# Kernel tuning notes

Measured on AMD Instinct MI355X. Metric: run time of the kernel, lower is better.

Reference implementation:

```python
import jax, jax.numpy as jnp
import numpy as np

B, N, C = 32, 2248, 1024
D = 128            # bottleneck (down_size)
P = 200            # num_prompt_tokens
SCALE = D ** (-0.5)


def setup_inputs() -> dict:
    key = jax.random.key(0)
    k = jax.random.split(key, 5)
    return {
        "x": jax.random.normal(k[0], (B, N, C), dtype=jnp.float32),
        "W_down": jax.random.normal(k[1], (C, D), dtype=jnp.float32) * (C ** -0.5),
        "b_down": jax.random.normal(k[2], (D,), dtype=jnp.float32) * 0.01,
        "W_up": jax.random.normal(k[3], (D, C), dtype=jnp.float32) * (D ** -0.5),
        "b_up": jax.random.normal(k[4], (C,), dtype=jnp.float32) * 0.01,
        "gate": jnp.ones((), dtype=jnp.float32),
    }


def reference(x, W_down, b_down, W_up, b_up, gate):
    # down-projection + exact GELU (torch nn.GELU default is erf-based)
    down = jax.nn.gelu(jnp.einsum('bnc,cd->bnd', x, W_down) + b_down,
                       approximate=False)                      # [B, N, D]
    prompt_down = down[:, :P, :]                               # [B, P, D]
    token_down = down[:, P:, :]                                # [B, N-P, D]
    # prompt-token cross attention
    attn = jax.nn.softmax(
        jnp.einsum('bpd,btd->bpt', prompt_down, token_down) * SCALE, axis=-1)
    prompt_out = jnp.einsum('bpt,btd->bpd', attn, token_down)  # [B, P, D]
    combined = jnp.concatenate([prompt_out, token_down], axis=1)  # [B, N, D]
    up = jnp.einsum('bnd,dc->bnc', combined, W_up) + b_up      # [B, N, C]
    return gate * up
```

## Files before the change

kernel.cpp:

```cpp
#include <hip/hip_runtime.h>
#include <hip/hip_bf16.h>
#include <math.h>

#define B_   32
#define N_   2248
#define C_   1024
#define D_   128
#define P_   200
#define T_   2048
#define M_   (B_ * N_)
#define SCALE_ 0.08838834764831845f

typedef __bf16 bf16;
typedef __bf16 bf16x8 __attribute__((ext_vector_type(8)));
typedef __bf16 bf16x4 __attribute__((ext_vector_type(4)));
typedef float  f32x4  __attribute__((ext_vector_type(4)));
typedef unsigned int u32x4 __attribute__((ext_vector_type(4)));

#define VT_COL(dd, t) ((((((t) >> 3) ^ (((dd) >> 3) & 7)) << 3)) | ((t) & 7))

__device__ __forceinline__ void gl_lds16(const void* g, void* l) {
    __builtin_amdgcn_global_load_lds(
        (const __attribute__((address_space(1))) unsigned int*)g,
        (__attribute__((address_space(3))) unsigned int*)l,
        16, 0, 0);
}

__global__ void k_prep(const float* __restrict__ Wd, const float* __restrict__ Wu,
                       bf16* __restrict__ WtD, bf16* __restrict__ WtU) {
    int i = blockIdx.x * 256 + threadIdx.x;
    if (i >= 131072) return;
    int d = i >> 10, k = i & 1023;
    WtD[i] = (bf16)Wd[k * 128 + d];
    int c = i >> 7, e = i & 127;
    WtU[i] = (bf16)Wu[e * 1024 + c];
}

__launch_bounds__(256, 3)
__global__ void k_down(const float* __restrict__ x, const bf16* __restrict__ WtD,
                       const float* __restrict__ bd, bf16* __restrict__ down) {
    __shared__ __align__(16) char ring[3][16384];
    const int tid = threadIdx.x;
    const int lane = tid & 63, w = tid >> 6;
    const int wm = w >> 1, wn = w & 1;
    const int li = lane & 15, lg = lane >> 4;
    const int m0 = blockIdx.x * 64;

    const int cA0 = w * 2, cA1 = w * 2 + 1;
    const int ar0 = cA0 * 8 + (lane >> 3);
    const int ar1 = cA1 * 8 + (lane >> 3);
    const float* asrc0 = x + (size_t)(m0 + ar0) * C_ + ((((lane & 7) ^ (ar0 & 7)) * 16) >> 2);
    const float* asrc1 = x + (size_t)(m0 + ar1) * C_ + ((((lane & 7) ^ (ar1 & 7)) * 16) >> 2);
    const int br0 = cA0 * 16 + (lane >> 2);
    const int br1 = cA1 * 16 + (lane >> 2);
    const bf16* bsrc0 = WtD + (size_t)br0 * C_ + (((lane & 3) ^ (br0 & 3)) * 8);
    const bf16* bsrc1 = WtD + (size_t)br1 * C_ + (((lane & 3) ^ (br1 & 3)) * 8);

#define STAGE_(t_, s_) do {                                              \
        gl_lds16(asrc0 + (t_) * 32, ring[s_] + cA0 * 1024);              \
        gl_lds16(asrc1 + (t_) * 32, ring[s_] + cA1 * 1024);              \
        gl_lds16(bsrc0 + (t_) * 32, ring[s_] + 8192 + cA0 * 1024);       \
        gl_lds16(bsrc1 + (t_) * 32, ring[s_] + 8192 + cA1 * 1024);       \
    } while (0)

    f32x4 acc[2][4];
    const f32x4 zero = {0.f, 0.f, 0.f, 0.f};
#pragma unroll
    for (int i = 0; i < 2; i++)
#pragma unroll
        for (int j = 0; j < 4; j++) acc[i][j] = zero;

    STAGE_(0, 0);
    STAGE_(1, 1);

    for (int t = 0; t < 32; t++) {
        if (t < 31) { asm volatile("s_waitcnt vmcnt(4)" ::: "memory"); }
        else        { asm volatile("s_waitcnt vmcnt(0)" ::: "memory"); }
        __builtin_amdgcn_sched_barrier(0);
        __builtin_amdgcn_s_barrier();
        __builtin_amdgcn_sched_barrier(0);
        if (t + 2 < 32) {
            int s = (t + 2) % 3;
            STAGE_(t + 2, s);
        }
        const char* sa = ring[t % 3];
        const char* sb = sa + 8192;
        bf16x8 af[2];
#pragma unroll
        for (int f = 0; f < 2; f++) {
            int row = wm * 32 + f * 16 + li;
            const char* rb = sa + row * 128;
            int p0 = (2 * lg) ^ (row & 7), p1 = (2 * lg + 1) ^ (row & 7);
            f32x4 a0 = *(const f32x4*)(rb + p0 * 16);
            f32x4 a1 = *(const f32x4*)(rb + p1 * 16);
            bf16x8 o;
            o[0] = (bf16)a0[0]; o[1] = (bf16)a0[1]; o[2] = (bf16)a0[2]; o[3] = (bf16)a0[3];
            o[4] = (bf16)a1[0]; o[5] = (bf16)a1[1]; o[6] = (bf16)a1[2]; o[7] = (bf16)a1[3];
            af[f] = o;
        }
        bf16x8 bfr[4];
#pragma unroll
        for (int f = 0; f < 4; f++) {
            int row = wn * 64 + f * 16 + li;
            bfr[f] = *(const bf16x8*)(sb + row * 64 + ((lg ^ (row & 3)) * 16));
        }
#pragma unroll
        for (int fm = 0; fm < 2; fm++)
#pragma unroll
            for (int fn = 0; fn < 4; fn++)
                acc[fm][fn] = __builtin_amdgcn_mfma_f32_16x16x32_bf16(
                    af[fm], bfr[fn], acc[fm][fn], 0, 0, 0);
    }
#undef STAGE_

#pragma unroll
    for (int fn = 0; fn < 4; fn++) {
        int col = wn * 64 + fn * 16 + li;
        float bias = bd[col];
#pragma unroll
        for (int fm = 0; fm < 2; fm++) {
            int rb = m0 + wm * 32 + fm * 16 + lg * 4;
#pragma unroll
            for (int r = 0; r < 4; r++) {
                float v = acc[fm][fn][r] + bias;
                float g = 0.5f * v * (1.0f + erff(v * 0.70710678118654752f));
                down[(size_t)(rb + r) * D_ + col] = (bf16)g;
            }
        }
    }
}

__launch_bounds__(256, 2)
__global__ void k_attn(const bf16* __restrict__ down, float* __restrict__ Opart,
                       float* __restrict__ Mpart, float* __restrict__ Lpart) {
    __shared__ bf16 Qs[64][136];
    __shared__ bf16 Ks[64][136];
    __shared__ bf16 Vt[128][72];
    __shared__ bf16 Ps[4][16][72];
    const int tid = threadIdx.x;
    const int lane = tid & 63, w = tid >> 6;
    const int li = lane & 15, lg = lane >> 4;
    const int bid = blockIdx.x;
    const int wg = (bid & 7) * 64 + (bid >> 3);
    const int b  = wg >> 4;
    const int qt = (wg >> 2) & 3;
    const int th = wg & 3;
    const size_t base = (size_t)b * N_ * D_;
    const int tbase = P_ + th * 512;

#pragma unroll
    for (int it = 0; it < 4; it++) {
        int ch = tid + it * 256;
        int r = ch >> 4, c8 = (ch & 15) * 8;
        *(u32x4*)&Qs[r][c8] = *(const u32x4*)(down + base + (size_t)(qt * 64 + r) * D_ + c8);
    }
    __syncthreads();
    bf16x8 qf[4];
#pragma unroll
    for (int kk = 0; kk < 4; kk++)
        qf[kk] = *(const bf16x8*)&Qs[w * 16 + li][kk * 32 + lg * 8];

    float m_run[4], l_run[4];
    f32x4 acc[8];
    const f32x4 zero = {0.f, 0.f, 0.f, 0.f};
#pragma unroll
    for (int r = 0; r < 4; r++) { m_run[r] = -3.0e38f; l_run[r] = 0.f; }
#pragma unroll
    for (int fn = 0; fn < 8; fn++) acc[fn] = zero;

    for (int tt = 0; tt < 8; tt++) {
        __syncthreads();
#pragma unroll
        for (int it = 0; it < 4; it++) {
            int ch = tid + it * 256;
            int r = ch >> 4, c8 = (ch & 15) * 8;
            u32x4 v = *(const u32x4*)(down + base + (size_t)(tbase + tt * 64 + r) * D_ + c8);
            *(u32x4*)&Ks[r][c8] = v;
            bf16 tmp[8];
            *(u32x4*)tmp = v;
#pragma unroll
            for (int j = 0; j < 8; j++) Vt[c8 + j][VT_COL(c8 + j, r)] = tmp[j];
        }
        __syncthreads();
        f32x4 s[4];
#pragma unroll
        for (int fn = 0; fn < 4; fn++) {
            s[fn] = zero;
#pragma unroll
            for (int kk = 0; kk < 4; kk++) {
                bf16x8 kf = *(const bf16x8*)&Ks[fn * 16 + li][kk * 32 + lg * 8];
                s[fn] = __builtin_amdgcn_mfma_f32_16x16x32_bf16(qf[kk], kf, s[fn], 0, 0, 0);
            }
            s[fn] *= SCALE_;
        }
#pragma unroll
        for (int r = 0; r < 4; r++) {
            float tmax = fmaxf(fmaxf(s[0][r], s[1][r]), fmaxf(s[2][r], s[3][r]));
#pragma unroll
            for (int off = 1; off < 16; off <<= 1)
                tmax = fmaxf(tmax, __shfl_xor(tmax, off, 64));
            float mnew = fmaxf(m_run[r], tmax);
            float corr = __expf(m_run[r] - mnew);
            m_run[r] = mnew;
            float psum = 0.f;
#pragma unroll
            for (int fn = 0; fn < 4; fn++) {
                float p = __expf(s[fn][r] - mnew);
                psum += p;
                Ps[w][lg * 4 + r][fn * 16 + li] = (bf16)p;
            }
#pragma unroll
            for (int off = 1; off < 16; off <<= 1)
                psum += __shfl_xor(psum, off, 64);
            l_run[r] = l_run[r] * corr + psum;
#pragma unroll
            for (int fn = 0; fn < 8; fn++) acc[fn][r] *= corr;
        }
#pragma unroll
        for (int kk = 0; kk < 2; kk++) {
            bf16x8 pf = *(const bf16x8*)&Ps[w][li][kk * 32 + lg * 8];
#pragma unroll
            for (int fn = 0; fn < 8; fn++) {
                int d = fn * 16 + li;
                bf16x8 vf = *(const bf16x8*)&Vt[d][VT_COL(d, kk * 32 + lg * 8)];
                acc[fn] = __builtin_amdgcn_mfma_f32_16x16x32_bf16(pf, vf, acc[fn], 0, 0, 0);
            }
        }
    }
#pragma unroll
    for (int r = 0; r < 4; r++) {
        int q = qt * 64 + w * 16 + lg * 4 + r;
        size_t ro = ((size_t)(b * 4 + th) * 256 + q) * 128;
#pragma unroll
        for (int fn = 0; fn < 8; fn++)
            Opart[ro + fn * 16 + li] = acc[fn][r];
        if (li == 0) {
            Mpart[(b * 4 + th) * 256 + q] = m_run[r];
            Lpart[(b * 4 + th) * 256 + q] = l_run[r];
        }
    }
}

__global__ void k_comb(const float* __restrict__ Opart, const float* __restrict__ Mpart,
                       const float* __restrict__ Lpart, bf16* __restrict__ pout) {
    int gid = blockIdx.x * 256 + threadIdx.x;
    if (gid >= (B_ * P_ * D_) / 4) return;
    int e = gid * 4;
    int row = e >> 7;
    int col = e & 127;
    int b = row / P_;
    int q = row - b * P_;
    float mm[4], ll[4];
    float m = -3.0e38f;
#pragma unroll
    for (int t = 0; t < 4; t++) {
        mm[t] = Mpart[(b * 4 + t) * 256 + q];
        ll[t] = Lpart[(b * 4 + t) * 256 + q];
        m = fmaxf(m, mm[t]);
    }
    float a[4], lsum = 0.f;
#pragma unroll
    for (int t = 0; t < 4; t++) { a[t] = __expf(mm[t] - m); lsum += ll[t] * a[t]; }
    float inv = 1.0f / lsum;
    f32x4 o = {0.f, 0.f, 0.f, 0.f};
#pragma unroll
    for (int t = 0; t < 4; t++) {
        f32x4 ot = *(const f32x4*)&Opart[((size_t)(b * 4 + t) * 256 + q) * 128 + col];
#pragma unroll
        for (int j = 0; j < 4; j++) o[j] += ot[j] * a[t];
    }
    bf16x4 ob;
#pragma unroll
    for (int j = 0; j < 4; j++) ob[j] = (bf16)(o[j] * inv);
    *(bf16x4*)&pout[(size_t)row * 128 + col] = ob;
}

__launch_bounds__(256, 3)
__global__ void k_up(const bf16* __restrict__ down, const bf16* __restrict__ pout,
                     const bf16* __restrict__ WtU, const float* __restrict__ bu,
                     const float* __restrict__ gate, float* __restrict__ out) {
    const int tid = threadIdx.x;
    const int lane = tid & 63, wid = tid >> 6;
    const int wm = wid >> 1, wn = wid & 1;
    const int li = lane & 15, lg = lane >> 4;
    int bid = blockIdx.x;
    int wg = (bid & 7) * 562 + (bid >> 3);
    const int mt = wg >> 3, nt = wg & 7;
    const int m0 = mt * 128, n0 = nt * 128;

    const bf16* rp[4];
#pragma unroll
    for (int f = 0; f < 4; f++) {
        int row = m0 + wm * 64 + f * 16 + li;
        int bb = row / N_;
        int n = row - bb * N_;
        rp[f] = (n < P_) ? (pout + (size_t)(bb * P_ + n) * D_ + lg * 8)
                         : (down + (size_t)row * D_ + lg * 8);
    }
    const bf16* Bp = WtU + (size_t)(n0 + wn * 64 + li) * D_ + lg * 8;

    f32x4 acc[4][4];
    const f32x4 zero = {0.f, 0.f, 0.f, 0.f};
#pragma unroll
    for (int i = 0; i < 4; i++)
#pragma unroll
        for (int j = 0; j < 4; j++) acc[i][j] = zero;

#pragma unroll
    for (int kk = 0; kk < 4; kk++) {
        bf16x8 af[4], bf_[4];
#pragma unroll
        for (int f = 0; f < 4; f++) {
            af[f]  = *(const bf16x8*)(rp[f] + kk * 32);
            bf_[f] = *(const bf16x8*)(Bp + (size_t)(f * 16) * D_ + kk * 32);
        }
#pragma unroll
        for (int fm = 0; fm < 4; fm++)
#pragma unroll
            for (int fn = 0; fn < 4; fn++)
                acc[fm][fn] = __builtin_amdgcn_mfma_f32_16x16x32_bf16(
                    af[fm], bf_[fn], acc[fm][fn], 0, 0, 0);
    }

    float g = gate[0];
#pragma unroll
    for (int fn = 0; fn < 4; fn++) {
        int c = n0 + wn * 64 + fn * 16 + li;
        float bias = bu[c];
#pragma unroll
        for (int fm = 0; fm < 4; fm++) {
            int rb = m0 + wm * 64 + fm * 16 + lg * 4;
#pragma unroll
            for (int r = 0; r < 4; r++)
                out[(size_t)(rb + r) * C_ + c] = g * (acc[fm][fn][r] + bias);
        }
    }
}

extern "C" void kernel_launch(void* const* d_in, const int* in_sizes, int n_in,
                              void* d_out, int out_size, void* d_ws, size_t ws_size,
                              hipStream_t stream) {
    const float* x    = (const float*)d_in[0];
    const float* Wd   = (const float*)d_in[1];
    const float* bd   = (const float*)d_in[2];
    const float* Wu   = (const float*)d_in[3];
    const float* bu   = (const float*)d_in[4];
    const float* gate = (const float*)d_in[5];
    float* out = (float*)d_out;

    char* w = (char*)d_ws;
    bf16*  down  = (bf16*)w;
    bf16*  pout  = (bf16*)(w + 18415616);
    bf16*  WtD   = (bf16*)(w + 20054016);
    bf16*  WtU   = (bf16*)(w + 20316160);
    float* Opart = (float*)(w + 20578304);
    float* Mpart = (float*)(w + 37355520);
    float* Lpart = (float*)(w + 37486592);

    k_prep<<<512, 256, 0, stream>>>(Wd, Wu, WtD, WtU);
    k_down<<<M_ / 64, 256, 0, stream>>>(x, WtD, bd, down);
    k_attn<<<512, 256, 0, stream>>>(down, Opart, Mpart, Lpart);
    k_comb<<<800, 256, 0, stream>>>(Opart, Mpart, Lpart, pout);
    k_up<<<(M_ / 128) * 8, 256, 0, stream>>>(down, pout, WtU, bu, gate, out);
}
```

Measured before the change: 236.1 us.

## Fuse attention with token up-projection and drop split-KV combine

Attention now runs one block per (batch, query tile) over the full token range, so the split-KV partials and the combine kernel are gone. The attention blocks share a launch with the up-projection for token rows, which do not depend on attention, so the two workloads overlap. Prompt rows are up-projected in a separate small kernel afterwards. This removes a launch and the fp32 partial traffic, but only 128 long-running attention blocks remain, and they may form a tail if they are not scheduled early.

```diff
diff --git a/kernel.cpp b/kernel.cpp
--- a/kernel.cpp
+++ b/kernel.cpp
@@ -130,172 +130,176 @@
     }
 }
 
-__launch_bounds__(256, 2)
-__global__ void k_attn(const bf16* __restrict__ down, float* __restrict__ Opart,
-                       float* __restrict__ Mpart, float* __restrict__ Lpart) {
-    __shared__ bf16 Qs[64][136];
+__launch_bounds__(256, 3)
+__global__ void k_fused(const bf16* __restrict__ down, bf16* __restrict__ pout,
+                        const bf16* __restrict__ WtU, const float* __restrict__ bu,
+                        const float* __restrict__ gate, float* __restrict__ out) {
     __shared__ bf16 Ks[64][136];
     __shared__ bf16 Vt[128][72];
     __shared__ bf16 Ps[4][16][72];
     const int tid = threadIdx.x;
     const int lane = tid & 63, w = tid >> 6;
     const int li = lane & 15, lg = lane >> 4;
-    const int bid = blockIdx.x;
-    const int wg = (bid & 7) * 64 + (bid >> 3);
-    const int b  = wg >> 4;
-    const int qt = (wg >> 2) & 3;
-    const int th = wg & 3;
-    const size_t base = (size_t)b * N_ * D_;
-    const int tbase = P_ + th * 512;
-
-#pragma unroll
-    for (int it = 0; it < 4; it++) {
-        int ch = tid + it * 256;
-        int r = ch >> 4, c8 = (ch & 15) * 8;
-        *(u32x4*)&Qs[r][c8] = *(const u32x4*)(down + base + (size_t)(qt * 64 + r) * D_ + c8);
-    }
-    __syncthreads();
-    bf16x8 qf[4];
-#pragma unroll
-    for (int kk = 0; kk < 4; kk++)
-        qf[kk] = *(const bf16x8*)&Qs[w * 16 + li][kk * 32 + lg * 8];
-
-    float m_run[4], l_run[4];
-    f32x4 acc[8];
-    const f32x4 zero = {0.f, 0.f, 0.f, 0.f};
-#pragma unroll
-    for (int r = 0; r < 4; r++) { m_run[r] = -3.0e38f; l_run[r] = 0.f; }
-#pragma unroll
-    for (int fn = 0; fn < 8; fn++) acc[fn] = zero;
-
-    for (int tt = 0; tt < 8; tt++) {
-        __syncthreads();
-#pragma unroll
-        for (int it = 0; it < 4; it++) {
-            int ch = tid + it * 256;
-            int r = ch >> 4, c8 = (ch & 15) * 8;
-            u32x4 v = *(const u32x4*)(down + base + (size_t)(tbase + tt * 64 + r) * D_ + c8);
-            *(u32x4*)&Ks[r][c8] = v;
-            bf16 tmp[8];
-            *(u32x4*)tmp = v;
-#pragma unroll
-            for (int j = 0; j < 8; j++) Vt[c8 + j][VT_COL(c8 + j, r)] = tmp[j];
-        }
-        __syncthreads();
-        f32x4 s[4];
+
+    if (blockIdx.x < 128) {
+        const int b  = blockIdx.x >> 2;
+        const int qt = blockIdx.x & 3;
+        const size_t base = (size_t)b * N_ * D_;
+
+        bf16x8 qf[4];
+#pragma unroll
+        for (int kk = 0; kk < 4; kk++)
+            qf[kk] = *(const bf16x8*)(down + base +
+                        (size_t)(qt * 64 + w * 16 + li) * D_ + kk * 32 + lg * 8);
+
+        float m_run[4], l_run[4];
+        f32x4 acc[8];
+        const f32x4 zero = {0.f, 0.f, 0.f, 0.f};
+#pragma unroll
+        for (int r = 0; r < 4; r++) { m_run[r] = -3.0e38f; l_run[r] = 0.f; }
+#pragma unroll
+        for (int fn = 0; fn < 8; fn++) acc[fn] = zero;
+
+        for (int tt = 0; tt < 32; tt++) {
+            __syncthreads();
+#pragma unroll
+            for (int it = 0; it < 4; it++) {
+                int ch = tid + it * 256;
+                int r = ch >> 4, c8 = (ch & 15) * 8;
+                u32x4 v = *(const u32x4*)(down + base +
+                              (size_t)(P_ + tt * 64 + r) * D_ + c8);
+                *(u32x4*)&Ks[r][c8] = v;
+                bf16 tmp[8];
+                *(u32x4*)tmp = v;
+#pragma unroll
+                for (int j = 0; j < 8; j++) Vt[c8 + j][VT_COL(c8 + j, r)] = tmp[j];
+            }
+            __syncthreads();
+            f32x4 s[4];
+#pragma unroll
+            for (int fn = 0; fn < 4; fn++) {
+                s[fn] = zero;
+#pragma unroll
+                for (int kk = 0; kk < 4; kk++) {
+                    bf16x8 kf = *(const bf16x8*)&Ks[fn * 16 + li][kk * 32 + lg * 8];
+                    s[fn] = __builtin_amdgcn_mfma_f32_16x16x32_bf16(qf[kk], kf, s[fn], 0, 0, 0);
+                }
+                s[fn] *= SCALE_;
+            }
+#pragma unroll
+            for (int r = 0; r < 4; r++) {
+                float tmax = fmaxf(fmaxf(s[0][r], s[1][r]), fmaxf(s[2][r], s[3][r]));
+#pragma unroll
+                for (int off = 1; off < 16; off <<= 1)
+                    tmax = fmaxf(tmax, __shfl_xor(tmax, off, 64));
+                float mnew = fmaxf(m_run[r], tmax);
+                float corr = __expf(m_run[r] - mnew);
+                m_run[r] = mnew;
+                float psum = 0.f;
+#pragma unroll
+                for (int fn = 0; fn < 4; fn++) {
+                    float p = __expf(s[fn][r] - mnew);
+                    psum += p;
+                    Ps[w][lg * 4 + r][fn * 16 + li] = (bf16)p;
+                }
+#pragma unroll
+                for (int off = 1; off < 16; off <<= 1)
+                    psum += __shfl_xor(psum, off, 64);
+                l_run[r] = l_run[r] * corr + psum;
+#pragma unroll
+                for (int fn = 0; fn < 8; fn++) acc[fn][r] *= corr;
+            }
+#pragma unroll
+            for (int kk = 0; kk < 2; kk++) {
+                bf16x8 pf = *(const bf16x8*)&Ps[w][li][kk * 32 + lg * 8];
+#pragma unroll
+                for (int fn = 0; fn < 8; fn++) {
+                    int d = fn * 16 + li;
+                    bf16x8 vf = *(const bf16x8*)&Vt[d][VT_COL(d, kk * 32 + lg * 8)];
+                    acc[fn] = __builtin_amdgcn_mfma_f32_16x16x32_bf16(pf, vf, acc[fn], 0, 0, 0);
+                }
+            }
+        }
+#pragma unroll
+        for (int r = 0; r < 4; r++) {
+            int q = qt * 64 + w * 16 + lg * 4 + r;
+            if (q < P_) {
+                float inv = 1.0f / l_run[r];
+#pragma unroll
+                for (int fn = 0; fn < 8; fn++)
+                    pout[(size_t)(b * P_ + q) * D_ + fn * 16 + li] = (bf16)(acc[fn][r] * inv);
+            }
+        }
+    } else {
+        const int wm = w >> 1, wn = w & 1;
+        int bidu = blockIdx.x - 128;
+        int wg = (bidu & 7) * 512 + (bidu >> 3);
+        const int b  = wg >> 7;
+        const int rt = (wg >> 3) & 15;
+        const int nt = wg & 7;
+        const size_t m0 = (size_t)b * N_ + P_ + rt * 128;
+        const int n0 = nt * 128;
+
+        const bf16* Bp = WtU + (size_t)(n0 + wn * 64 + li) * D_ + lg * 8;
+
+        f32x4 acc[4][4];
+        const f32x4 zero = {0.f, 0.f, 0.f, 0.f};
+#pragma unroll
+        for (int i = 0; i < 4; i++)
+#pragma unroll
+            for (int j = 0; j < 4; j++) acc[i][j] = zero;
+
+#pragma unroll
+        for (int kk = 0; kk < 4; kk++) {
+            bf16x8 af[4], bf_[4];
+#pragma unroll
+            for (int f = 0; f < 4; f++) {
+                af[f]  = *(const bf16x8*)(down + (m0 + wm * 64 + f * 16 + li) * D_ + kk * 32 + lg * 8);
+                bf_[f] = *(const bf16x8*)(Bp + (size_t)(f * 16) * D_ + kk * 32);
+            }
+#pragma unroll
+            for (int fm = 0; fm < 4; fm++)
+#pragma unroll
+                for (int fn = 0; fn < 4; fn++)
+                    acc[fm][fn] = __builtin_amdgcn_mfma_f32_16x16x32_bf16(
+                        af[fm], bf_[fn], acc[fm][fn], 0, 0, 0);
+        }
+
+        float g = gate[0];
 #pragma unroll
         for (int fn = 0; fn < 4; fn++) {
-            s[fn] = zero;
-#pragma unroll
-            for (int kk = 0; kk < 4; kk++) {
-                bf16x8 kf = *(const bf16x8*)&Ks[fn * 16 + li][kk * 32 + lg * 8];
-                s[fn] = __builtin_amdgcn_mfma_f32_16x16x32_bf16(qf[kk], kf, s[fn], 0, 0, 0);
-            }
-            s[fn] *= SCALE_;
-        }
-#pragma unroll
-        for (int r = 0; r < 4; r++) {
-            float tmax = fmaxf(fmaxf(s[0][r], s[1][r]), fmaxf(s[2][r], s[3][r]));
-#pragma unroll
-            for (int off = 1; off < 16; off <<= 1)
-                tmax = fmaxf(tmax, __shfl_xor(tmax, off, 64));
-            float mnew = fmaxf(m_run[r], tmax);
-            float corr = __expf(m_run[r] - mnew);
-            m_run[r] = mnew;
-            float psum = 0.f;
-#pragma unroll
-            for (int fn = 0; fn < 4; fn++) {
-                float p = __expf(s[fn][r] - mnew);
-                psum += p;
-                Ps[w][lg * 4 + r][fn * 16 + li] = (bf16)p;
-            }
-#pragma unroll
-            for (int off = 1; off < 16; off <<= 1)
-                psum += __shfl_xor(psum, off, 64);
-            l_run[r] = l_run[r] * corr + psum;
-#pragma unroll
-            for (int fn = 0; fn < 8; fn++) acc[fn][r] *= corr;
-        }
-#pragma unroll
-        for (int kk = 0; kk < 2; kk++) {
-            bf16x8 pf = *(const bf16x8*)&Ps[w][li][kk * 32 + lg * 8];
-#pragma unroll
-            for (int fn = 0; fn < 8; fn++) {
-                int d = fn * 16 + li;
-                bf16x8 vf = *(const bf16x8*)&Vt[d][VT_COL(d, kk * 32 + lg * 8)];
-                acc[fn] = __builtin_amdgcn_mfma_f32_16x16x32_bf16(pf, vf, acc[fn], 0, 0, 0);
-            }
-        }
-    }
-#pragma unroll
-    for (int r = 0; r < 4; r++) {
-        int q = qt * 64 + w * 16 + lg * 4 + r;
-        size_t ro = ((size_t)(b * 4 + th) * 256 + q) * 128;
-#pragma unroll
-        for (int fn = 0; fn < 8; fn++)
-            Opart[ro + fn * 16 + li] = acc[fn][r];
-        if (li == 0) {
-            Mpart[(b * 4 + th) * 256 + q] = m_run[r];
-            Lpart[(b * 4 + th) * 256 + q] = l_run[r];
-        }
-    }
-}
-
-__global__ void k_comb(const float* __restrict__ Opart, const float* __restrict__ Mpart,
-                       const float* __restrict__ Lpart, bf16* __restrict__ pout) {
-    int gid = blockIdx.x * 256 + threadIdx.x;
-    if (gid >= (B_ * P_ * D_) / 4) return;
-    int e = gid * 4;
-    int row = e >> 7;
-    int col = e & 127;
-    int b = row / P_;
-    int q = row - b * P_;
-    float mm[4], ll[4];
-    float m = -3.0e38f;
-#pragma unroll
-    for (int t = 0; t < 4; t++) {
-        mm[t] = Mpart[(b * 4 + t) * 256 + q];
-        ll[t] = Lpart[(b * 4 + t) * 256 + q];
-        m = fmaxf(m, mm[t]);
-    }
-    float a[4], lsum = 0.f;
-#pragma unroll
-    for (int t = 0; t < 4; t++) { a[t] = __expf(mm[t] - m); lsum += ll[t] * a[t]; }
-    float inv = 1.0f / lsum;
-    f32x4 o = {0.f, 0.f, 0.f, 0.f};
-#pragma unroll
-    for (int t = 0; t < 4; t++) {
-        f32x4 ot = *(const f32x4*)&Opart[((size_t)(b * 4 + t) * 256 + q) * 128 + col];
-#pragma unroll
-        for (int j = 0; j < 4; j++) o[j] += ot[j] * a[t];
-    }
-    bf16x4 ob;
-#pragma unroll
-    for (int j = 0; j < 4; j++) ob[j] = (bf16)(o[j] * inv);
-    *(bf16x4*)&pout[(size_t)row * 128 + col] = ob;
+            int c = n0 + wn * 64 + fn * 16 + li;
+            float bias = bu[c];
+#pragma unroll
+            for (int fm = 0; fm < 4; fm++) {
+                size_t rb = m0 + wm * 64 + fm * 16 + lg * 4;
+#pragma unroll
+                for (int r = 0; r < 4; r++)
+                    out[(rb + r) * C_ + c] = g * (acc[fm][fn][r] + bias);
+            }
+        }
+    }
 }
 
 __launch_bounds__(256, 3)
-__global__ void k_up(const bf16* __restrict__ down, const bf16* __restrict__ pout,
-                     const bf16* __restrict__ WtU, const float* __restrict__ bu,
-                     const float* __restrict__ gate, float* __restrict__ out) {
+__global__ void k_up_prompt(const bf16* __restrict__ pout, const bf16* __restrict__ WtU,
+                            const float* __restrict__ bu, const float* __restrict__ gate,
+                            float* __restrict__ out) {
     const int tid = threadIdx.x;
     const int lane = tid & 63, wid = tid >> 6;
     const int wm = wid >> 1, wn = wid & 1;
     const int li = lane & 15, lg = lane >> 4;
-    int bid = blockIdx.x;
-    int wg = (bid & 7) * 562 + (bid >> 3);
-    const int mt = wg >> 3, nt = wg & 7;
-    const int m0 = mt * 128, n0 = nt * 128;
+    const int b  = blockIdx.x >> 4;
+    const int pt = (blockIdx.x >> 3) & 1;
+    const int nt = blockIdx.x & 7;
+    const int n0 = nt * 128;
 
     const bf16* rp[4];
 #pragma unroll
     for (int f = 0; f < 4; f++) {
-        int row = m0 + wm * 64 + f * 16 + li;
-        int bb = row / N_;
-        int n = row - bb * N_;
-        rp[f] = (n < P_) ? (pout + (size_t)(bb * P_ + n) * D_ + lg * 8)
-                         : (down + (size_t)row * D_ + lg * 8);
+        int n = pt * 128 + wm * 64 + f * 16 + li;
+        int nc = n < P_ ? n : P_ - 1;
+        rp[f] = pout + (size_t)(b * P_ + nc) * D_ + lg * 8;
     }
     const bf16* Bp = WtU + (size_t)(n0 + wn * 64 + li) * D_ + lg * 8;
 
@@ -329,10 +333,12 @@
         float bias = bu[c];
 #pragma unroll
         for (int fm = 0; fm < 4; fm++) {
-            int rb = m0 + wm * 64 + fm * 16 + lg * 4;
-#pragma unroll
-            for (int r = 0; r < 4; r++)
-                out[(size_t)(rb + r) * C_ + c] = g * (acc[fm][fn][r] + bias);
+            int nr = pt * 128 + wm * 64 + fm * 16 + lg * 4;
+#pragma unroll
+            for (int r = 0; r < 4; r++) {
+                if (nr + r < P_)
+                    out[((size_t)b * N_ + nr + r) * C_ + c] = g * (acc[fm][fn][r] + bias);
+            }
         }
     }
 }
@@ -349,17 +355,13 @@
     float* out = (float*)d_out;
 
     char* w = (char*)d_ws;
-    bf16*  down  = (bf16*)w;
-    bf16*  pout  = (bf16*)(w + 18415616);
-    bf16*  WtD   = (bf16*)(w + 20054016);
-    bf16*  WtU   = (bf16*)(w + 20316160);
-    float* Opart = (float*)(w + 20578304);
-    float* Mpart = (float*)(w + 37355520);
-    float* Lpart = (float*)(w + 37486592);
+    bf16* down = (bf16*)w;
+    bf16* pout = (bf16*)(w + 18415616);
+    bf16* WtD  = (bf16*)(w + 20054016);
+    bf16* WtU  = (bf16*)(w + 20316160);
 
     k_prep<<<512, 256, 0, stream>>>(Wd, Wu, WtD, WtU);
     k_down<<<M_ / 64, 256, 0, stream>>>(x, WtD, bd, down);
-    k_attn<<<512, 256, 0, stream>>>(down, Opart, Mpart, Lpart);
-    k_comb<<<800, 256, 0, stream>>>(Opart, Mpart, Lpart, pout);
-    k_up<<<(M_ / 128) * 8, 256, 0, stream>>>(down, pout, WtU, bu, gate, out);
-}
+    k_fused<<<128 + 4096, 256, 0, stream>>>(down, pout, WtU, bu, gate, out);
+    k_up_prompt<<<512, 256, 0, stream>>>(pout, WtU, bu, gate, out);
+}
```

Result: slower. 271.1 us (+14.8%).
